# Kernel tuning notes

Hardware: AMD Instinct MI355X
Metric: run time of the kernel (lower is better)

The kernel has to match this reference:

```python
import jax, jax.numpy as jnp
import numpy as np

N = 50000        # nodes
E = 800000       # edges
G = 64           # graphs in batch
IN = 128         # node_in_channels
H = 128          # hidden_channels
OUT = 1


def setup_inputs() -> dict:
    key = jax.random.key(0)
    ks = jax.random.split(key, 12)
    x = jax.random.normal(ks[0], (N, IN), jnp.float32)
    edge_index = jax.random.randint(ks[1], (2, E), 0, N, dtype=jnp.int64)
    batch = jnp.sort(jax.random.randint(ks[2], (N,), 0, G, dtype=jnp.int64))

    def glorot(k, fan_in, fan_out):
        s = jnp.sqrt(2.0 / (fan_in + fan_out)).astype(jnp.float32)
        return jax.random.normal(k, (fan_in, fan_out), jnp.float32) * s

    return {
        "x": x, "edge_index": edge_index, "batch": batch,
        "W1": glorot(ks[3], IN, H), "b1": jnp.zeros((H,), jnp.float32),
        "W2": glorot(ks[4], H, H),  "b2": jnp.zeros((H,), jnp.float32),
        "W3": glorot(ks[5], H, H),  "b3": jnp.zeros((H,), jnp.float32),
        "Wf1": glorot(ks[6], 2 * H, H), "bf1": jnp.zeros((H,), jnp.float32),
        "Wf2": glorot(ks[7], H, OUT),   "bf2": jnp.zeros((OUT,), jnp.float32),
    }


def reference(x, edge_index, batch, W1, b1, W2, b2, W3, b3, Wf1, bf1, Wf2, bf2):
    src, dst = edge_index[0], edge_index[1]
    # GCN symmetric normalization with self-loops: deg counts in-edges + self-loop
    deg = 1.0 + jax.ops.segment_sum(jnp.ones((E,), x.dtype), dst, num_segments=N)
    dis = jax.lax.rsqrt(deg)                       # deg >= 1, safe
    edge_norm = (dis[src] * dis[dst])[:, None]     # [E, 1]
    self_norm = (dis * dis)[:, None]               # [N, 1] self-loop weight

    def gcn_conv(h, W, b):
        h = h @ W                                   # [N, H]
        agg = jax.ops.segment_sum(h[src] * edge_norm, dst, num_segments=N)
        return agg + h * self_norm + b

    h = jax.nn.relu(gcn_conv(x, W1, b1))   # dropout = identity (eval mode)
    h = jax.nn.relu(gcn_conv(h, W2, b2))
    h = jax.nn.relu(gcn_conv(h, W3, b3))

    counts = jax.ops.segment_sum(jnp.ones((N,), h.dtype), batch, num_segments=G)
    x_mean = jax.ops.segment_sum(h, batch, num_segments=G) / jnp.maximum(counts, 1.0)[:, None]
    x_max = jax.ops.segment_max(h, batch, num_segments=G)
    x_max = jnp.where(jnp.isfinite(x_max), x_max, 0.0)  # guard empty graphs
    pooled = jnp.concatenate([x_mean, x_max], axis=1)    # [G, 2H]

    hidden = jax.nn.relu(pooled @ Wf1 + bf1)
    return hidden @ Wf2 + bf2                            # [G, 1]
```

## Files before the change

### kernel.cpp

```cpp
#include <hip/hip_runtime.h>

#define HD 128
#define PS 32

typedef __bf16 bf16x8 __attribute__((ext_vector_type(8)));
typedef float  f32x16 __attribute__((ext_vector_type(16)));
typedef unsigned short u16x4 __attribute__((ext_vector_type(4)));
typedef _Float16 f16x4 __attribute__((ext_vector_type(4)));

__device__ inline unsigned short f2bf_rne(float f) {
  unsigned u = __builtin_bit_cast(unsigned, f);
  unsigned r = u + 0x7fffu + ((u >> 16) & 1u);
  return (unsigned short)(r >> 16);
}
__device__ inline float bf2f(unsigned short h) {
  unsigned u = ((unsigned)h) << 16;
  return __builtin_bit_cast(float, u);
}
__device__ inline void cvt4(float4 f, u16x4& h, u16x4& l) {
  h[0] = f2bf_rne(f.x); l[0] = f2bf_rne(f.x - bf2f(h[0]));
  h[1] = f2bf_rne(f.y); l[1] = f2bf_rne(f.y - bf2f(h[1]));
  h[2] = f2bf_rne(f.z); l[2] = f2bf_rne(f.z - bf2f(h[2]));
  h[3] = f2bf_rne(f.w); l[3] = f2bf_rne(f.w - bf2f(h[3]));
}

__global__ __launch_bounds__(256) void k_prep(const float* __restrict__ x, unsigned short* __restrict__ ph,
                                              unsigned short* __restrict__ pl, int nelem4,
                                              const float* __restrict__ W1, const float* __restrict__ W2,
                                              const float* __restrict__ W3, unsigned short* __restrict__ wimg,
                                              int* __restrict__ cnt, int n, int nbX,
                                              int* __restrict__ gstart, int* __restrict__ gend, int g) {
  int b = blockIdx.x;
  int t = threadIdx.x;
  if (b < nbX) {
    int i = b * 256 + t;
    if (i < nelem4) {
      float4 f = ((const float4*)x)[i];
      u16x4 h, l;
      cvt4(f, h, l);
      ((u16x4*)ph)[i] = h;
      ((u16x4*)pl)[i] = l;
    }
  } else if (b < nbX + 51) {
    int wb = b - nbX;
    const float* W = (wb < 17) ? W1 : (wb < 34) ? W2 : W3;
    unsigned short* out = wimg + (size_t)(wb / 17) * 34816;
    int base = ((wb % 17) * 256 + t) * 4;
#pragma unroll
    for (int p = 0; p < 4; ++p) {
      int flat = base + p;
      int c = flat / 136, j = flat - c * 136;
      float v = (j < 128) ? W[(size_t)j * HD + c] : 0.f;
      unsigned short hi = f2bf_rne(v);
      float lo = (j < 128) ? (v - bf2f(hi)) : 0.f;
      out[(size_t)c * 136 + j] = hi;
      out[17408 + (size_t)c * 136 + j] = f2bf_rne(lo);
    }
  } else {
    int bb = b - nbX - 51;
    int i = bb * 256 + t;
    if (i < n) cnt[i] = 0;
    if (bb == 0 && t < g) { gstart[t] = 0x7fffffff; gend[t] = -1; }
  }
}

__global__ __launch_bounds__(256) void k_hist(const int* __restrict__ dst, int* __restrict__ cnt,
                                              int* __restrict__ eslot, int e) {
  int i = blockIdx.x * 256 + threadIdx.x;
  if (i < e) eslot[i] = atomicAdd(&cnt[dst[i]], 1);
}

__global__ __launch_bounds__(256) void k_scan1(const int* __restrict__ cnt, int* __restrict__ excl,
                                               int* __restrict__ bsum, int n) {
  __shared__ int s[256];
  int tid = threadIdx.x;
  int i = blockIdx.x * 256 + tid;
  int v = (i < n) ? cnt[i] : 0;
  s[tid] = v; __syncthreads();
  for (int off = 1; off < 256; off <<= 1) {
    int t = (tid >= off) ? s[tid - off] : 0;
    __syncthreads();
    s[tid] += t;
    __syncthreads();
  }
  if (i < n) excl[i] = s[tid] - v;
  if (tid == 255) bsum[blockIdx.x] = s[255];
}

__global__ __launch_bounds__(256) void k_finalize(int* __restrict__ rowptr, const int* __restrict__ bsum,
                                                  const int* __restrict__ cnt, float* __restrict__ dis,
                                                  const int* __restrict__ batch, int* __restrict__ gstart,
                                                  int* __restrict__ gend, int n) {
  __shared__ int spre;
  int tid = threadIdx.x;
  int nb = blockIdx.x;
  if (tid < 64) {
    int acc = 0;
    for (int j = tid; j < nb; j += 64) acc += bsum[j];
#pragma unroll
    for (int m = 1; m < 64; m <<= 1) acc += __shfl_xor(acc, m);
    if (tid == 0) spre = acc;
  }
  __syncthreads();
  int pre = spre;
  int i = nb * 256 + tid;
  if (i >= n) return;
  rowptr[i] += pre;
  dis[i] = rsqrtf(1.0f + (float)cnt[i]);
  int b = batch[i];
  if (i == 0 || batch[i - 1] != b) gstart[b] = i;
  if (i == n - 1 || batch[i + 1] != b) gend[b] = i;
}

__global__ __launch_bounds__(256) void k_fill(const int* __restrict__ src, const int* __restrict__ dst,
                                              const int* __restrict__ rowptr, const int* __restrict__ eslot,
                                              int* __restrict__ csr, int e) {
  int i = blockIdx.x * 256 + threadIdx.x;
  if (i >= e) return;
  csr[rowptr[dst[i]] + eslot[i]] = src[i];
}

__global__ __launch_bounds__(1024) void k_gemm(const unsigned short* __restrict__ AH,
                                               const unsigned short* __restrict__ AL,
                                               const unsigned short* __restrict__ wimg_l,
                                               const float* __restrict__ rowscale,
                                               _Float16* __restrict__ C, int M) {
  __shared__ unsigned short alds[2][128][136];
  __shared__ unsigned short wlds[2][128][136];
  int t = threadIdx.x;
  int row0 = blockIdx.x * 128;
  char* ab = (char*)alds;
  char* wb = (char*)wlds;
  const int PL = 128 * 272;

  {
    const float4* sH = (const float4*)(AH + (size_t)row0 * HD);
    const float4* sL = (const float4*)(AL + (size_t)row0 * HD);
#pragma unroll
    for (int u = 0; u < 2; ++u) {
      int s = u * 1024 + t;
      int r = s >> 4, c = s & 15;
      *(float4*)(ab + r * 272 + c * 16) = sH[s];
      *(float4*)(ab + PL + r * 272 + c * 16) = sL[s];
    }
  }
  {
    const float4* sW = (const float4*)wimg_l;
    float4* dW = (float4*)wb;
#pragma unroll
    for (int u = 0; u < 4; ++u) dW[u * 1024 + t] = sW[u * 1024 + t];
    if (t < 256) dW[4096 + t] = sW[4096 + t];
  }
  __syncthreads();

  int w = t >> 6, lane = t & 63;
  int l31 = lane & 31, lhi = lane >> 5;
  int wr = (w >> 2) * 32, wc = (w & 3) * 32;

  f32x16 acc;
#pragma unroll
  for (int i = 0; i < 16; ++i) acc[i] = 0.f;

#pragma unroll
  for (int ks = 0; ks < 8; ++ks) {
    int ko = ks * 32 + lhi * 16;
    bf16x8 ah = *(const bf16x8*)(ab + (wr + l31) * 272 + ko);
    bf16x8 al = *(const bf16x8*)(ab + PL + (wr + l31) * 272 + ko);
    bf16x8 bh = *(const bf16x8*)(wb + (wc + l31) * 272 + ko);
    bf16x8 bl = *(const bf16x8*)(wb + PL + (wc + l31) * 272 + ko);
    acc = __builtin_amdgcn_mfma_f32_32x32x16_bf16(ah, bh, acc, 0, 0, 0);
    acc = __builtin_amdgcn_mfma_f32_32x32x16_bf16(ah, bl, acc, 0, 0, 0);
    acc = __builtin_amdgcn_mfma_f32_32x32x16_bf16(al, bh, acc, 0, 0, 0);
  }

  int col = wc + l31;
  int rbase = row0 + wr + 4 * lhi;
#pragma unroll
  for (int r = 0; r < 16; ++r) {
    int row = rbase + (r & 3) + 8 * (r >> 2);
    if (row < M) C[(size_t)row * HD + col] = (_Float16)(rowscale[row] * acc[r]);
  }
}

__global__ __launch_bounds__(256) void k_gather(const _Float16* __restrict__ C, const float* __restrict__ dis,
                                                const int* __restrict__ rowptr, const int* __restrict__ cnt,
                                                const int* __restrict__ csr, const float* __restrict__ bias,
                                                float* __restrict__ outF, unsigned short* __restrict__ outH,
                                                unsigned short* __restrict__ outL, int n) {
  int lane = threadIdx.x & 63;
  int wid = threadIdx.x >> 6;
  int half = lane >> 5;
  int l32 = lane & 31;
  int node = blockIdx.x * 8 + wid * 2 + half;
  if (node >= n) return;
  int coff = l32 * 4;
  int s = rowptr[node];
  int deg = cnt[node];

  float dn = dis[node];
  f16x4 sh = *(const f16x4*)(C + (size_t)node * HD + coff);
  float4 bb = *(const float4*)(bias + coff);

  float4 a0 = make_float4(0.f, 0.f, 0.f, 0.f);
  float4 a1 = a0, a2 = a0, a3 = a0;
  int i = 0;
  for (; i + 4 <= deg; i += 4) {
    int i0 = csr[s + i];
    int i1 = csr[s + i + 1];
    int i2 = csr[s + i + 2];
    int i3 = csr[s + i + 3];
    f16x4 v0 = *(const f16x4*)(C + (size_t)i0 * HD + coff);
    f16x4 v1 = *(const f16x4*)(C + (size_t)i1 * HD + coff);
    f16x4 v2 = *(const f16x4*)(C + (size_t)i2 * HD + coff);
    f16x4 v3 = *(const f16x4*)(C + (size_t)i3 * HD + coff);
    a0.x += (float)v0[0]; a0.y += (float)v0[1]; a0.z += (float)v0[2]; a0.w += (float)v0[3];
    a1.x += (float)v1[0]; a1.y += (float)v1[1]; a1.z += (float)v1[2]; a1.w += (float)v1[3];
    a2.x += (float)v2[0]; a2.y += (float)v2[1]; a2.z += (float)v2[2]; a2.w += (float)v2[3];
    a3.x += (float)v3[0]; a3.y += (float)v3[1]; a3.z += (float)v3[2]; a3.w += (float)v3[3];
  }
  for (; i < deg; ++i) {
    int i0 = csr[s + i];
    f16x4 v0 = *(const f16x4*)(C + (size_t)i0 * HD + coff);
    a0.x += (float)v0[0]; a0.y += (float)v0[1]; a0.z += (float)v0[2]; a0.w += (float)v0[3];
  }
  a0.x += a1.x + a2.x + a3.x;
  a0.y += a1.y + a2.y + a3.y;
  a0.z += a1.z + a2.z + a3.z;
  a0.w += a1.w + a2.w + a3.w;

  float4 r;
  r.x = fmaxf(dn * (a0.x + (float)sh[0]) + bb.x, 0.f);
  r.y = fmaxf(dn * (a0.y + (float)sh[1]) + bb.y, 0.f);
  r.z = fmaxf(dn * (a0.z + (float)sh[2]) + bb.z, 0.f);
  r.w = fmaxf(dn * (a0.w + (float)sh[3]) + bb.w, 0.f);
  if (outF) {
    *(float4*)(outF + (size_t)node * HD + coff) = r;
  } else {
    u16x4 h, l;
    cvt4(r, h, l);
    *(u16x4*)(outH + (size_t)node * HD + coff) = h;
    *(u16x4*)(outL + (size_t)node * HD + coff) = l;
  }
}

__global__ __launch_bounds__(128) void k_pool1(const float* __restrict__ h, const int* __restrict__ gstart,
                                               const int* __restrict__ gend, float* __restrict__ psum,
                                               float* __restrict__ pmax) {
  int g = blockIdx.x, sidx = blockIdx.y, c = threadIdx.x;
  int s = gstart[g], e = gend[g];
  float sum = 0.f, mx = 0.f;
  if (s <= e) {
    int len = e - s + 1;
    int c0 = s + (int)(((long long)len * sidx) / PS);
    int c1 = s + (int)(((long long)len * (sidx + 1)) / PS);
    for (int i = c0; i < c1; ++i) {
      float v = h[(size_t)i * HD + c];
      sum += v;
      mx = fmaxf(mx, v);
    }
  }
  size_t o = ((size_t)g * PS + sidx) * HD + c;
  psum[o] = sum;
  pmax[o] = mx;
}

__global__ __launch_bounds__(128) void k_pool2mlp(const float* __restrict__ psum, const float* __restrict__ pmax,
                                                  const int* __restrict__ gstart, const int* __restrict__ gend,
                                                  const float* __restrict__ Wf1, const float* __restrict__ bf1,
                                                  const float* __restrict__ Wf2, const float* __restrict__ bf2,
                                                  float* __restrict__ out) {
  __shared__ float p[256];
  __shared__ float red[128];
  int g = blockIdx.x, t = threadIdx.x;
  float sum = 0.f, mx = 0.f;
  for (int sidx = 0; sidx < PS; ++sidx) {
    size_t o = ((size_t)g * PS + sidx) * HD + t;
    sum += psum[o];
    mx = fmaxf(mx, pmax[o]);
  }
  int s = gstart[g], e = gend[g];
  float cntf = (s <= e) ? (float)(e - s + 1) : 1.0f;
  p[t] = sum / cntf;
  p[t + 128] = mx;
  __syncthreads();
  float acc = bf1[t];
  for (int k = 0; k < 256; ++k) acc += p[k] * Wf1[k * HD + t];
  float hv = fmaxf(acc, 0.f);
  red[t] = hv * Wf2[t];
  __syncthreads();
  for (int off = 64; off > 0; off >>= 1) {
    if (t < off) red[t] += red[t + off];
    __syncthreads();
  }
  if (t == 0) out[g] = red[0] + bf2[0];
}

extern "C" void kernel_launch(void* const* d_in, const int* in_sizes, int n_in,
                              void* d_out, int out_size, void* d_ws, size_t ws_size,
                              hipStream_t stream) {
  const float* x   = (const float*)d_in[0];
  const int*   ei  = (const int*)d_in[1];
  const int*   bat = (const int*)d_in[2];
  const float* W1  = (const float*)d_in[3];
  const float* b1  = (const float*)d_in[4];
  const float* W2  = (const float*)d_in[5];
  const float* b2  = (const float*)d_in[6];
  const float* W3  = (const float*)d_in[7];
  const float* b3  = (const float*)d_in[8];
  const float* Wf1 = (const float*)d_in[9];
  const float* bf1 = (const float*)d_in[10];
  const float* Wf2 = (const float*)d_in[11];
  const float* bf2 = (const float*)d_in[12];

  int N = in_sizes[0] / HD;
  int E = in_sizes[1] / 2;
  int G = out_size;

  int gb = (N + 127) / 128;
  int Rpad = gb * 128;

  char* w = (char*)d_ws;
  size_t off = 0;
  auto alloc = [&](size_t bytes) -> void* {
    void* p = w + off;
    off = (off + bytes + 255) & ~(size_t)255;
    return p;
  };
  unsigned short* pH0 = (unsigned short*)alloc((size_t)Rpad * HD * 2);
  unsigned short* pL0 = (unsigned short*)alloc((size_t)Rpad * HD * 2);
  unsigned short* pH1 = (unsigned short*)alloc((size_t)Rpad * HD * 2);
  unsigned short* pL1 = (unsigned short*)alloc((size_t)Rpad * HD * 2);
  _Float16* Cbuf = (_Float16*)alloc((size_t)Rpad * HD * 2);
  float* Hf     = (float*)alloc((size_t)N * HD * 4);
  int*   csr    = (int*)alloc((size_t)E * 4);
  int*   cnt    = (int*)alloc((size_t)N * 4);
  int*   rowptr = (int*)alloc((size_t)N * 4);
  float* dis    = (float*)alloc((size_t)N * 4);
  int*   bsum   = (int*)alloc(256 * 4);
  int*   gstart = (int*)alloc((size_t)G * 4);
  int*   gend   = (int*)alloc((size_t)G * 4);
  float* psum   = (float*)alloc((size_t)G * PS * HD * 4);
  float* pmax   = (float*)alloc((size_t)G * PS * HD * 4);
  unsigned short* wimg = (unsigned short*)alloc((size_t)3 * 34816 * 2);
  int*   eslot  = (int*)Hf;

  int nbN = (N + 255) / 256;
  int nbE = (E + 255) / 256;
  int nelem4 = N * HD / 4;
  int nbX = (nelem4 + 255) / 256;

  k_prep<<<nbX + 51 + nbN, 256, 0, stream>>>(x, pH0, pL0, nelem4, W1, W2, W3, wimg, cnt, N, nbX,
                                             gstart, gend, G);
  k_hist<<<nbE, 256, 0, stream>>>(ei + E, cnt, eslot, E);
  k_scan1<<<nbN, 256, 0, stream>>>(cnt, rowptr, bsum, N);
  k_finalize<<<nbN, 256, 0, stream>>>(rowptr, bsum, cnt, dis, bat, gstart, gend, N);
  k_fill<<<nbE, 256, 0, stream>>>(ei, ei + E, rowptr, eslot, csr, E);

  int ab = (N + 7) / 8;
  k_gemm<<<gb, 1024, 0, stream>>>(pH0, pL0, wimg, dis, Cbuf, N);
  k_gather<<<ab, 256, 0, stream>>>(Cbuf, dis, rowptr, cnt, csr, b1, nullptr, pH1, pL1, N);
  k_gemm<<<gb, 1024, 0, stream>>>(pH1, pL1, wimg + 34816, dis, Cbuf, N);
  k_gather<<<ab, 256, 0, stream>>>(Cbuf, dis, rowptr, cnt, csr, b2, nullptr, pH0, pL0, N);
  k_gemm<<<gb, 1024, 0, stream>>>(pH0, pL0, wimg + 69632, dis, Cbuf, N);
  k_gather<<<ab, 256, 0, stream>>>(Cbuf, dis, rowptr, cnt, csr, b3, Hf, nullptr, nullptr, N);

  dim3 pgrid(G, PS);
  k_pool1<<<pgrid, 128, 0, stream>>>(Hf, gstart, gend, psum, pmax);
  k_pool2mlp<<<G, 128, 0, stream>>>(psum, pmax, gstart, gend, Wf1, bf1, Wf2, bf2, (float*)d_out);
}
```

Baseline: 236.4 us.

## Fuse edge histogram into first GEMM and move degree scaling out of GEMM

The first GEMM no longer depends on the degree normalization. It now runs before the CSR build and also does the in-degree atomic histogram in a grid-stride loop, so the separate histogram kernel is gone. Degree scaling moves into the gather: layer 1 weights each neighbor by dis[src]. Later layers pre-scale their output by dis before the bf16 split, so the GEMM epilogue drops the rowscale load. This removes one launch and a per-row load in the epilogue, but adds a per-neighbor dis load in the first gather and stretches the first GEMM with atomic work.

Result: faster. 218.4 us (-7.6%).

```diff
diff --git a/kernel.cpp b/kernel.cpp
--- a/kernel.cpp
+++ b/kernel.cpp
@@ -64,12 +64,6 @@
   }
 }
 
-__global__ __launch_bounds__(256) void k_hist(const int* __restrict__ dst, int* __restrict__ cnt,
-                                              int* __restrict__ eslot, int e) {
-  int i = blockIdx.x * 256 + threadIdx.x;
-  if (i < e) eslot[i] = atomicAdd(&cnt[dst[i]], 1);
-}
-
 __global__ __launch_bounds__(256) void k_scan1(const int* __restrict__ cnt, int* __restrict__ excl,
                                                int* __restrict__ bsum, int n) {
   __shared__ int s[256];
@@ -123,8 +117,9 @@
 __global__ __launch_bounds__(1024) void k_gemm(const unsigned short* __restrict__ AH,
                                                const unsigned short* __restrict__ AL,
                                                const unsigned short* __restrict__ wimg_l,
-                                               const float* __restrict__ rowscale,
-                                               _Float16* __restrict__ C, int M) {
+                                               _Float16* __restrict__ C, int M,
+                                               const int* __restrict__ hdst, int* __restrict__ hcnt,
+                                               int* __restrict__ heslot, int hE) {
   __shared__ unsigned short alds[2][128][136];
   __shared__ unsigned short wlds[2][128][136];
   int t = threadIdx.x;
@@ -178,10 +173,17 @@
 #pragma unroll
   for (int r = 0; r < 16; ++r) {
     int row = rbase + (r & 3) + 8 * (r >> 2);
-    if (row < M) C[(size_t)row * HD + col] = (_Float16)(rowscale[row] * acc[r]);
-  }
-}
-
+    if (row < M) C[(size_t)row * HD + col] = (_Float16)acc[r];
+  }
+
+  if (hdst) {
+    int stride = gridDim.x * 1024;
+    for (int i = blockIdx.x * 1024 + t; i < hE; i += stride)
+      heslot[i] = atomicAdd(&hcnt[hdst[i]], 1);
+  }
+}
+
+template <bool L1>
 __global__ __launch_bounds__(256) void k_gather(const _Float16* __restrict__ C, const float* __restrict__ dis,
                                                 const int* __restrict__ rowptr, const int* __restrict__ cnt,
                                                 const int* __restrict__ csr, const float* __restrict__ bias,
@@ -213,31 +215,36 @@
     f16x4 v1 = *(const f16x4*)(C + (size_t)i1 * HD + coff);
     f16x4 v2 = *(const f16x4*)(C + (size_t)i2 * HD + coff);
     f16x4 v3 = *(const f16x4*)(C + (size_t)i3 * HD + coff);
-    a0.x += (float)v0[0]; a0.y += (float)v0[1]; a0.z += (float)v0[2]; a0.w += (float)v0[3];
-    a1.x += (float)v1[0]; a1.y += (float)v1[1]; a1.z += (float)v1[2]; a1.w += (float)v1[3];
-    a2.x += (float)v2[0]; a2.y += (float)v2[1]; a2.z += (float)v2[2]; a2.w += (float)v2[3];
-    a3.x += (float)v3[0]; a3.y += (float)v3[1]; a3.z += (float)v3[2]; a3.w += (float)v3[3];
+    float w0 = 1.f, w1 = 1.f, w2 = 1.f, w3 = 1.f;
+    if (L1) { w0 = dis[i0]; w1 = dis[i1]; w2 = dis[i2]; w3 = dis[i3]; }
+    a0.x += w0 * (float)v0[0]; a0.y += w0 * (float)v0[1]; a0.z += w0 * (float)v0[2]; a0.w += w0 * (float)v0[3];
+    a1.x += w1 * (float)v1[0]; a1.y += w1 * (float)v1[1]; a1.z += w1 * (float)v1[2]; a1.w += w1 * (float)v1[3];
+    a2.x += w2 * (float)v2[0]; a2.y += w2 * (float)v2[1]; a2.z += w2 * (float)v2[2]; a2.w += w2 * (float)v2[3];
+    a3.x += w3 * (float)v3[0]; a3.y += w3 * (float)v3[1]; a3.z += w3 * (float)v3[2]; a3.w += w3 * (float)v3[3];
   }
   for (; i < deg; ++i) {
     int i0 = csr[s + i];
     f16x4 v0 = *(const f16x4*)(C + (size_t)i0 * HD + coff);
-    a0.x += (float)v0[0]; a0.y += (float)v0[1]; a0.z += (float)v0[2]; a0.w += (float)v0[3];
+    float w0 = L1 ? dis[i0] : 1.f;
+    a0.x += w0 * (float)v0[0]; a0.y += w0 * (float)v0[1]; a0.z += w0 * (float)v0[2]; a0.w += w0 * (float)v0[3];
   }
   a0.x += a1.x + a2.x + a3.x;
   a0.y += a1.y + a2.y + a3.y;
   a0.z += a1.z + a2.z + a3.z;
   a0.w += a1.w + a2.w + a3.w;
 
+  float ss = L1 ? dn : 1.f;
   float4 r;
-  r.x = fmaxf(dn * (a0.x + (float)sh[0]) + bb.x, 0.f);
-  r.y = fmaxf(dn * (a0.y + (float)sh[1]) + bb.y, 0.f);
-  r.z = fmaxf(dn * (a0.z + (float)sh[2]) + bb.z, 0.f);
-  r.w = fmaxf(dn * (a0.w + (float)sh[3]) + bb.w, 0.f);
+  r.x = fmaxf(dn * (a0.x + ss * (float)sh[0]) + bb.x, 0.f);
+  r.y = fmaxf(dn * (a0.y + ss * (float)sh[1]) + bb.y, 0.f);
+  r.z = fmaxf(dn * (a0.z + ss * (float)sh[2]) + bb.z, 0.f);
+  r.w = fmaxf(dn * (a0.w + ss * (float)sh[3]) + bb.w, 0.f);
   if (outF) {
     *(float4*)(outF + (size_t)node * HD + coff) = r;
   } else {
+    float4 rs = make_float4(dn * r.x, dn * r.y, dn * r.z, dn * r.w);
     u16x4 h, l;
-    cvt4(r, h, l);
+    cvt4(rs, h, l);
     *(u16x4*)(outH + (size_t)node * HD + coff) = h;
     *(u16x4*)(outL + (size_t)node * HD + coff) = l;
   }
@@ -351,18 +358,17 @@
 
   k_prep<<<nbX + 51 + nbN, 256, 0, stream>>>(x, pH0, pL0, nelem4, W1, W2, W3, wimg, cnt, N, nbX,
                                              gstart, gend, G);
-  k_hist<<<nbE, 256, 0, stream>>>(ei + E, cnt, eslot, E);
+  k_gemm<<<gb, 1024, 0, stream>>>(pH0, pL0, wimg, Cbuf, N, ei + E, cnt, eslot, E);
   k_scan1<<<nbN, 256, 0, stream>>>(cnt, rowptr, bsum, N);
   k_finalize<<<nbN, 256, 0, stream>>>(rowptr, bsum, cnt, dis, bat, gstart, gend, N);
   k_fill<<<nbE, 256, 0, stream>>>(ei, ei + E, rowptr, eslot, csr, E);
 
   int ab = (N + 7) / 8;
-  k_gemm<<<gb, 1024, 0, stream>>>(pH0, pL0, wimg, dis, Cbuf, N);
-  k_gather<<<ab, 256, 0, stream>>>(Cbuf, dis, rowptr, cnt, csr, b1, nullptr, pH1, pL1, N);
-  k_gemm<<<gb, 1024, 0, stream>>>(pH1, pL1, wimg + 34816, dis, Cbuf, N);
-  k_gather<<<ab, 256, 0, stream>>>(Cbuf, dis, rowptr, cnt, csr, b2, nullptr, pH0, pL0, N);
-  k_gemm<<<gb, 1024, 0, stream>>>(pH0, pL0, wimg + 69632, dis, Cbuf, N);
-  k_gather<<<ab, 256, 0, stream>>>(Cbuf, dis, rowptr, cnt, csr, b3, Hf, nullptr, nullptr, N);
+  k_gather<true><<<ab, 256, 0, stream>>>(Cbuf, dis, rowptr, cnt, csr, b1, nullptr, pH1, pL1, N);
+  k_gemm<<<gb, 1024, 0, stream>>>(pH1, pL1, wimg + 34816, Cbuf, N, nullptr, nullptr, nullptr, 0);
+  k_gather<false><<<ab, 256, 0, stream>>>(Cbuf, dis, rowptr, cnt, csr, b2, nullptr, pH0, pL0, N);
+  k_gemm<<<gb, 1024, 0, stream>>>(pH0, pL0, wimg + 69632, Cbuf, N, nullptr, nullptr, nullptr, 0);
+  k_gather<false><<<ab, 256, 0, stream>>>(Cbuf, dis, rowptr, cnt, csr, b3, Hf, nullptr, nullptr, N);
 
   dim3 pgrid(G, PS);
   k_pool1<<<pgrid, 128, 0, stream>>>(Hf, gstart, gend, psum, pmax);
```
